# Kernel optimization log

Hardware: AMD Instinct MI355X
Metric: run time of the kernel (lower is better)

Reference implementation:

```python
import jax, jax.numpy as jnp
import numpy as np

N_NODES = 24576
N_EDGES = 294912
B_GRAPHS = 128
D_IN = 92
D = 512
H = 8
HD = D // H
L = 3
DFF = 4 * D
LN_EPS = 1e-5


def _layer_norm(x, g, b):
    mu = jnp.mean(x, axis=-1, keepdims=True)
    var = jnp.mean((x - mu) ** 2, axis=-1, keepdims=True)
    return (x - mu) * jax.lax.rsqrt(var + LN_EPS) * g + b


def setup_inputs() -> dict:
    key = jax.random.key(0)
    ks = jax.random.split(key, 24)
    s = 0.02
    inp = {
        "node_features": jax.random.normal(ks[0], (N_NODES, D_IN), jnp.float32),
        "edge_index": jax.random.randint(ks[1], (2, N_EDGES), 0, N_NODES, jnp.int64),
        "edge_attr": jax.random.uniform(ks[2], (N_EDGES,), jnp.float32),
        "batch": jnp.sort(jax.random.randint(ks[3], (N_NODES,), 0, B_GRAPHS, jnp.int64)),
        # atom embedding Linear(92 -> D)
        "emb_w": jax.random.normal(ks[4], (D, D_IN), jnp.float32) * s,
        "emb_b": jnp.zeros((D,), jnp.float32),
        # per-layer MHA params (stacked over L layers)
        "in_proj_w": jax.random.normal(ks[5], (L, 3 * D, D), jnp.float32) * s,
        "in_proj_b": jnp.zeros((L, 3 * D), jnp.float32),
        "out_w": jax.random.normal(ks[6], (L, D, D), jnp.float32) * s,
        "out_b": jnp.zeros((L, D), jnp.float32),
        "ln1_g": jnp.ones((L, D), jnp.float32),
        "ln1_b": jnp.zeros((L, D), jnp.float32),
        "ffn_w1": jax.random.normal(ks[7], (L, DFF, D), jnp.float32) * s,
        "ffn_b1": jnp.zeros((L, DFF), jnp.float32),
        "ffn_w2": jax.random.normal(ks[8], (L, D, DFF), jnp.float32) * s,
        "ffn_b2": jnp.zeros((L, D), jnp.float32),
        "ln2_g": jnp.ones((L, D), jnp.float32),
        "ln2_b": jnp.zeros((L, D), jnp.float32),
        # output head: Linear(D,D) -> SiLU -> Linear(D,1)
        "head_w1": jax.random.normal(ks[9], (D, D), jnp.float32) * s,
        "head_b1": jnp.zeros((D,), jnp.float32),
        "head_w2": jax.random.normal(ks[10], (1, D), jnp.float32) * s,
        "head_b2": jnp.zeros((1,), jnp.float32),
    }
    return inp


def _forward(node_features, batch, emb_w, emb_b, in_proj_w, in_proj_b, out_w,
             out_b, ln1_g, ln1_b, ffn_w1, ffn_b1, ffn_w2, ffn_b2, ln2_g,
             ln2_b, head_w1, head_b1, head_w2, head_b2):
    N = node_features.shape[0]
    B = int(jnp.max(batch)) + 1
    counts = jnp.bincount(batch, length=B)            # (B,) nodes per graph
    S = int(jnp.max(counts))                          # max_nodes
    starts = jnp.searchsorted(batch, jnp.arange(B))   # batch is sorted
    pos = jnp.arange(N) - starts[batch]               # slot within graph

    h = node_features @ emb_w.T + emb_b               # (N, D)
    # ragged -> dense pad  (B, S, D)
    hp = jnp.zeros((B, S, D), h.dtype).at[batch, pos].set(h)
    key_pad = jnp.arange(S)[None, :] >= counts[:, None]   # True = padding

    scale = 1.0 / jnp.sqrt(jnp.asarray(HD, hp.dtype))
    for l in range(L):
        qkv = hp @ in_proj_w[l].T + in_proj_b[l]      # (B, S, 3D)
        q, k, v = jnp.split(qkv, 3, axis=-1)
        q = q.reshape(B, S, H, HD).transpose(0, 2, 1, 3)
        k = k.reshape(B, S, H, HD).transpose(0, 2, 1, 3)
        v = v.reshape(B, S, H, HD).transpose(0, 2, 1, 3)
        scores = jnp.einsum('bhqd,bhkd->bhqk', q, k) * scale
        scores = jnp.where(key_pad[:, None, None, :], -jnp.inf, scores)
        attn = jax.nn.softmax(scores, axis=-1)
        o = jnp.einsum('bhqk,bhkd->bhqd', attn, v)
        o = o.transpose(0, 2, 1, 3).reshape(B, S, D)
        o = o @ out_w[l].T + out_b[l]
        x = _layer_norm(hp + o, ln1_g[l], ln1_b[l])   # post-norm
        f = jax.nn.relu(x @ ffn_w1[l].T + ffn_b1[l]) @ ffn_w2[l].T + ffn_b2[l]
        hp = _layer_norm(x + f, ln2_g[l], ln2_b[l])

    # unpad + segment mean pool
    h_out = hp[batch, pos]                            # (N, D)
    pooled = jax.ops.segment_sum(h_out, batch, num_segments=B)
    pooled = pooled / counts[:, None].astype(pooled.dtype)
    y = jax.nn.silu(pooled @ head_w1.T + head_b1) @ head_w2.T + head_b2
    return y                                          # (B, 1)


def reference(node_features, edge_index, edge_attr, batch, emb_w, emb_b,
              in_proj_w, in_proj_b, out_w, out_b, ln1_g, ln1_b, ffn_w1,
              ffn_b1, ffn_w2, ffn_b2, ln2_g, ln2_b, head_w1, head_b1,
              head_w2, head_b2):
    # edge_index / edge_attr are accepted but unused, matching the torch forward
    return _forward(node_features, batch, emb_w, emb_b, in_proj_w, in_proj_b,
                    out_w, out_b, ln1_g, ln1_b, ffn_w1, ffn_b1, ffn_w2,
                    ffn_b2, ln2_g, ln2_b, head_w1, head_b1, head_w2, head_b2)
```

## Files before the change

### kernel.cpp

```cpp
#include <hip/hip_runtime.h>
#include <hip/hip_bf16.h>
#include <cstdint>
#include <cfloat>
#include <cstddef>
#include <type_traits>

#define N_NODES 24576
#define B_GRAPHS 128
#define D_IN 92
#define D_INP 96
#define DMODEL 512
#define NHEAD 8
#define HDIM 64
#define NLAYER 3
#define DFF 2048

typedef __attribute__((ext_vector_type(8))) short short8;
typedef __attribute__((ext_vector_type(4))) short short4v;
typedef __attribute__((ext_vector_type(8))) unsigned short ushort8;
typedef __attribute__((ext_vector_type(4))) float f32x4;

__device__ __forceinline__ float b2f(unsigned short u) {
  union { unsigned int i; float f; } x;
  x.i = ((unsigned int)u) << 16;
  return x.f;
}
__device__ __forceinline__ unsigned short f2b(float f) {
  __hip_bfloat16 h = __float2bfloat16(f);
  return *reinterpret_cast<unsigned short*>(&h);
}

__device__ __forceinline__ void gl2lds16(const __hip_bfloat16* g,
                                         __hip_bfloat16* l) {
  __builtin_amdgcn_global_load_lds(
      (const __attribute__((address_space(1))) unsigned int*)g,
      (__attribute__((address_space(3))) unsigned int*)l, 16, 0, 0);
}

__global__ void starts_k(const int* __restrict__ batch32, int* __restrict__ starts) {
  __shared__ int is64_s;
  const int tid = threadIdx.x;
  if (tid == 0) is64_s = 0;
  __syncthreads();
  int bad = 0;
  for (int i = tid; i < N_NODES - 1; i += 256)
    if (batch32[i] > batch32[i + 1]) bad = 1;
  if (bad) atomicOr(&is64_s, 1);
  __syncthreads();
  const int is64 = is64_s;
  if (tid <= B_GRAPHS) {
    int lo = 0, hi = N_NODES;
    while (lo < hi) {
      int mid = (lo + hi) >> 1;
      int v = is64 ? batch32[2 * mid] : batch32[mid];
      if (v < tid) lo = mid + 1; else hi = mid;
    }
    starts[tid] = lo;
  }
}

__global__ __launch_bounds__(256) void cvt_k(const float* __restrict__ in,
                                             __hip_bfloat16* __restrict__ out,
                                             int count4) {
  int i = blockIdx.x * 256 + threadIdx.x;
  if (i < count4) {
    float4 v = ((const float4*)in)[i];
    short4v o;
    o[0] = (short)f2b(v.x); o[1] = (short)f2b(v.y);
    o[2] = (short)f2b(v.z); o[3] = (short)f2b(v.w);
    ((short4v*)out)[i] = o;
  }
}

__global__ __launch_bounds__(256) void padcvt_k(const float* __restrict__ in,
                                                __hip_bfloat16* __restrict__ out,
                                                int rows) {
  int idx = blockIdx.x * 256 + threadIdx.x;
  if (idx < rows * D_INP) {
    int r = idx / D_INP, c = idx - r * D_INP;
    out[idx] = __float2bfloat16(c < D_IN ? in[(size_t)r * D_IN + c] : 0.0f);
  }
}

__global__ __launch_bounds__(256) void mgemm_k(
    const __hip_bfloat16* __restrict__ A, const __hip_bfloat16* __restrict__ W,
    const float* __restrict__ bias, const __hip_bfloat16* __restrict__ res,
    __hip_bfloat16* __restrict__ C, int M, int N, int K, int act) {
  __shared__ __align__(16) __hip_bfloat16 As[3][128 * 32];
  __shared__ __align__(16) __hip_bfloat16 Ws[3][128 * 32];
  const int tid = threadIdx.x;
  const int wave = tid >> 6, lane = tid & 63;

  const int nxt = N >> 7, nmt = M >> 7;
  int rowt, colt;
  if ((nmt & 7) == 0) {
    const int rows_per = nmt >> 3;
    const int x = blockIdx.x & 7;
    const int j = blockIdx.x >> 3;
    rowt = x * rows_per + j % rows_per;
    colt = j / rows_per;
  } else {
    rowt = blockIdx.x / nxt;
    colt = blockIdx.x % nxt;
  }
  const int m0 = rowt * 128, n0 = colt * 128;

  const int mw = (wave >> 1) * 64, nw = (wave & 1) * 64;
  const int quad = lane >> 4, l16 = lane & 15;

  f32x4 acc[4][4] = {};

  const int srow = wave * 32 + (lane >> 2);
  const int skc = (((lane & 3) + ((lane >> 2) >> 1)) & 3) * 8;
  const __hip_bfloat16* gA = A + (size_t)(m0 + srow) * K + skc;
  const __hip_bfloat16* gW = W + (size_t)(n0 + srow) * K + skc;
  const int lo = wave * 32 * 32;

  const int niter = K >> 5;
  gl2lds16(gA, &As[0][lo]);
  gl2lds16(gA + (size_t)16 * K, &As[0][lo + 16 * 32]);
  gl2lds16(gW, &Ws[0][lo]);
  gl2lds16(gW + (size_t)16 * K, &Ws[0][lo + 16 * 32]);
  if (niter > 1) {
    gl2lds16(gA + 32, &As[1][lo]);
    gl2lds16(gA + (size_t)16 * K + 32, &As[1][lo + 16 * 32]);
    gl2lds16(gW + 32, &Ws[1][lo]);
    gl2lds16(gW + (size_t)16 * K + 32, &Ws[1][lo + 16 * 32]);
  }

  const int prd = ((quad - (l16 >> 1)) & 3) * 8;

  for (int it = 0; it < niter; ++it) {
    if (it + 1 < niter)
      asm volatile("s_waitcnt vmcnt(4)\n\ts_barrier" ::: "memory");
    else
      asm volatile("s_waitcnt vmcnt(0)\n\ts_barrier" ::: "memory");
    if (it + 2 < niter) {
      const int kpre = (it + 2) * 32;
      const int nb = (it + 2) % 3;
      gl2lds16(gA + kpre, &As[nb][lo]);
      gl2lds16(gA + (size_t)16 * K + kpre, &As[nb][lo + 16 * 32]);
      gl2lds16(gW + kpre, &Ws[nb][lo]);
      gl2lds16(gW + (size_t)16 * K + kpre, &Ws[nb][lo + 16 * 32]);
    }
    const int cb = it % 3;
    short8 af[4], bf[4];
#pragma unroll
    for (int t = 0; t < 4; t++) {
      af[t] = *(const short8*)&As[cb][(mw + t * 16 + l16) * 32 + prd];
      bf[t] = *(const short8*)&Ws[cb][(nw + t * 16 + l16) * 32 + prd];
    }
#pragma unroll
    for (int mt = 0; mt < 4; mt++)
#pragma unroll
      for (int nt = 0; nt < 4; nt++)
        acc[mt][nt] = __builtin_amdgcn_mfma_f32_16x16x32_bf16(
            af[mt], bf[nt], acc[mt][nt], 0, 0, 0);
  }

  __syncthreads();
  float* eps = ((wave < 2) ? (float*)As : (float*)Ws) + (wave & 1) * (32 * 68);
  const int erow = lane >> 3;
  const int ec = (lane & 7) * 8;
#pragma unroll
  for (int pass = 0; pass < 2; pass++) {
#pragma unroll
    for (int mh = 0; mh < 2; mh++) {
      const int mt = pass * 2 + mh;
#pragma unroll
      for (int nt = 0; nt < 4; nt++) {
        const float bv = bias[n0 + nw + nt * 16 + l16];
#pragma unroll
        for (int i = 0; i < 4; i++)
          eps[(mh * 16 + quad * 4 + i) * 68 + nt * 16 + l16] =
              acc[mt][nt][i] + bv;
      }
    }
    asm volatile("s_waitcnt lgkmcnt(0)" ::: "memory");
#pragma unroll
    for (int j = 0; j < 4; j++) {
      const int r = j * 8 + erow;
      const int m = m0 + mw + pass * 32 + r;
      const int n = n0 + nw + ec;
      f32x4 v0 = *(const f32x4*)&eps[r * 68 + ec];
      f32x4 v1 = *(const f32x4*)&eps[r * 68 + ec + 4];
      float v[8] = {v0[0], v0[1], v0[2], v0[3], v1[0], v1[1], v1[2], v1[3]};
      if (res) {
        ushort8 rv = *(const ushort8*)((const unsigned short*)res +
                                       (size_t)m * N + n);
#pragma unroll
        for (int t = 0; t < 8; t++) v[t] += b2f(rv[t]);
      }
      ushort8 o;
#pragma unroll
      for (int t = 0; t < 8; t++) {
        float x = (act == 1) ? fmaxf(v[t], 0.0f) : v[t];
        o[t] = f2b(x);
      }
      *(ushort8*)((unsigned short*)C + (size_t)m * N + n) = o;
    }
    asm volatile("s_waitcnt lgkmcnt(0)" ::: "memory");
  }
}

__global__ __launch_bounds__(256) void gemm_k(
    const float* __restrict__ A, const float* __restrict__ W,
    const float* __restrict__ bias, const float* __restrict__ res,
    float* __restrict__ C, int M, int N, int K, int act) {
  __shared__ float As[16][68];
  __shared__ float Ws[16][68];
  const int tid = threadIdx.x;
  const int tx = tid & 15, ty = tid >> 4;
  const int m0 = blockIdx.y * 64, n0 = blockIdx.x * 64;
  const int lr = tid >> 2;
  const int lk = (tid & 3) * 4;
  float acc[4][4] = {{0.f}};
  for (int k0 = 0; k0 < K; k0 += 16) {
#pragma unroll
    for (int i = 0; i < 4; i++) {
      int k = k0 + lk + i;
      As[lk + i][lr] = (k < K) ? A[(size_t)(m0 + lr) * K + k] : 0.0f;
      Ws[lk + i][lr] = (k < K) ? W[(size_t)(n0 + lr) * K + k] : 0.0f;
    }
    __syncthreads();
#pragma unroll
    for (int kk = 0; kk < 16; kk++) {
      float4 a4 = *(const float4*)&As[kk][ty * 4];
      float4 w4 = *(const float4*)&Ws[kk][tx * 4];
      float a[4] = {a4.x, a4.y, a4.z, a4.w};
      float w[4] = {w4.x, w4.y, w4.z, w4.w};
#pragma unroll
      for (int i = 0; i < 4; i++)
#pragma unroll
        for (int j = 0; j < 4; j++) acc[i][j] += a[i] * w[j];
    }
    __syncthreads();
  }
#pragma unroll
  for (int i = 0; i < 4; i++) {
    int m = m0 + ty * 4 + i;
#pragma unroll
    for (int j = 0; j < 4; j++) {
      int n = n0 + tx * 4 + j;
      float v = acc[i][j] + bias[n];
      if (res) v += res[(size_t)m * N + n];
      if (act == 1) v = fmaxf(v, 0.0f);
      else if (act == 2) v = v / (1.0f + __expf(-v));
      C[(size_t)m * N + n] = v;
    }
  }
}

__global__ __launch_bounds__(256) void lnb_k(
    const __hip_bfloat16* __restrict__ in, const float* __restrict__ g,
    const float* __restrict__ b, __hip_bfloat16* __restrict__ out) {
  int row = blockIdx.x * 4 + (threadIdx.x >> 6);
  int lane = threadIdx.x & 63;
  const unsigned short* rp =
      (const unsigned short*)in + (size_t)row * DMODEL + lane * 8;
  ushort8 sv = *(const ushort8*)rp;
  float v[8];
  float s = 0.f;
#pragma unroll
  for (int i = 0; i < 8; i++) { v[i] = b2f(sv[i]); s += v[i]; }
#pragma unroll
  for (int off = 32; off; off >>= 1) s += __shfl_xor(s, off);
  float mu = s * (1.0f / DMODEL);
  float vs = 0.f;
#pragma unroll
  for (int i = 0; i < 8; i++) { float d = v[i] - mu; vs += d * d; }
#pragma unroll
  for (int off = 32; off; off >>= 1) vs += __shfl_xor(vs, off);
  float rs = rsqrtf(vs * (1.0f / DMODEL) + 1e-5f);
  ushort8 o;
#pragma unroll
  for (int i = 0; i < 8; i++) {
    int c = lane * 8 + i;
    o[i] = f2b((v[i] - mu) * rs * g[c] + b[c]);
  }
  *(ushort8*)((unsigned short*)out + (size_t)row * DMODEL + lane * 8) = o;
}

#define MAXNH 128
__global__ __launch_bounds__(256, 3) void attn5_k(
    const __hip_bfloat16* __restrict__ qkv, const int* __restrict__ starts,
    __hip_bfloat16* __restrict__ O1, __hip_bfloat16* __restrict__ O2,
    float* __restrict__ ml) {
  const int half = blockIdx.x & 1;
  const int gh = blockIdx.x >> 1;
  const int g = gh >> 3, h = gh & 7;
  int s0 = starts[g], s1 = starts[g + 1];
  s0 = min(max(s0, 0), N_NODES);
  s1 = min(max(s1, s0), N_NODES);
  const int n = s1 - s0, start = s0;
  if (n == 0) return;
  const int tid = threadIdx.x, wave = tid >> 6, lane = tid & 63;
  const int quad = lane >> 4, l16 = lane & 15;
  unsigned short* Oh = (unsigned short*)(half ? O2 : O1);

  __shared__ __align__(16) unsigned short Ks[128][72];
  __shared__ __align__(16) unsigned short Vt[64][136];
  __shared__ __align__(16) unsigned short Ps[4][16][136];

  if (n <= 2 * MAXNH) {
    const int nh1 = (n + 1) >> 1;
    const int k0g = half * nh1;
    const int nh = half ? (n - nh1) : nh1;
    const int ktq = (n + 15) >> 4;

    if (nh == 0) {
      for (int mt = wave; mt < ktq; mt += 4) {
        const int q = mt * 16 + l16;
        if (q < n) {
          short4v z = {0, 0, 0, 0};
#pragma unroll
          for (int dt = 0; dt < 4; dt++)
            *(short4v*)(Oh + (size_t)(start + q) * DMODEL + h * HDIM +
                        dt * 16 + quad * 4) = z;
          if (quad == 0) {
            float2 mlv = {-FLT_MAX, 0.0f};
            *(float2*)(ml + ((size_t)(start + q) * NHEAD + h) * 4 + half * 2) = mlv;
          }
        }
      }
      return;
    }

    for (int idx = tid; idx < nh * 8; idx += 256) {
      int r = idx >> 3, c = (idx & 7) * 8;
      *(ushort8*)&Ks[r][c] = *(const ushort8*)((const unsigned short*)qkv +
                                               (size_t)(start + k0g + r) * 1536 +
                                               512 + h * HDIM + c);
    }
    for (int idx = tid; idx < 16 * 8; idx += 256) {
      int r = nh + (idx >> 3), c = (idx & 7) * 8;
      if (r < 128) {
        ushort8 z = {0, 0, 0, 0, 0, 0, 0, 0};
        *(ushort8*)&Ks[r][c] = z;
      }
    }
    const int vr = tid & 31, dc8 = tid >> 5;
    for (int r0 = 0; r0 < nh; r0 += 32) {
      int r = r0 + vr;
      if (r < nh) {
        ushort8 v = *(const ushort8*)((const unsigned short*)qkv +
                                      (size_t)(start + k0g + r) * 1536 + 1024 +
                                      h * HDIM + dc8 * 8);
#pragma unroll
        for (int j = 0; j < 8; j++) Vt[dc8 * 8 + j][r] = v[j];
      }
    }
    for (int idx = tid; idx < 64 * 32; idx += 256) {
      int d = idx >> 5, r = nh + (idx & 31);
      if (r < 136) Vt[d][r] = 0;
    }
    __syncthreads();

    const int ktmax2 = (nh + 15) >> 4;
    const int nkc2 = (nh + 31) >> 5;
    const float scale = 0.125f;

    for (int mt = wave; mt < ktq; mt += 4) {
      const int qrow = start + min(mt * 16 + l16, n - 1);
      const short8 qf0 = *(const short8*)((const unsigned short*)qkv +
                                          (size_t)qrow * 1536 + h * HDIM + quad * 8);
      const short8 qf1 = *(const short8*)((const unsigned short*)qkv +
                                          (size_t)qrow * 1536 + h * HDIM + 32 + quad * 8);
      f32x4 sacc[8];
#pragma unroll
      for (int kt = 0; kt < 8; kt++) {
        if (kt < ktmax2) {
          const int krow = kt * 16 + l16;
          const short8 kf0 = *(const short8*)&Ks[krow][quad * 8];
          const short8 kf1 = *(const short8*)&Ks[krow][32 + quad * 8];
          f32x4 a = {0.f, 0.f, 0.f, 0.f};
          a = __builtin_amdgcn_mfma_f32_16x16x32_bf16(kf0, qf0, a, 0, 0, 0);
          a = __builtin_amdgcn_mfma_f32_16x16x32_bf16(kf1, qf1, a, 0, 0, 0);
          sacc[kt] = a;
        }
      }
      float mx = -FLT_MAX;
#pragma unroll
      for (int kt = 0; kt < 8; kt++) {
        if (kt < ktmax2) {
#pragma unroll
          for (int i = 0; i < 4; i++) {
            const int key = kt * 16 + quad * 4 + i;
            const float v = sacc[kt][i] * scale;
            sacc[kt][i] = v;
            if (key < nh) mx = fmaxf(mx, v);
          }
        }
      }
      mx = fmaxf(mx, __shfl_xor(mx, 16));
      mx = fmaxf(mx, __shfl_xor(mx, 32));
      float ls = 0.f;
#pragma unroll
      for (int kt = 0; kt < 8; kt++) {
        if (kt < ktmax2) {
#pragma unroll
          for (int i = 0; i < 4; i++) {
            const int key = kt * 16 + quad * 4 + i;
            const float p = (key < nh) ? __expf(sacc[kt][i] - mx) : 0.0f;
            sacc[kt][i] = p;
            ls += p;
          }
        }
      }
      ls += __shfl_xor(ls, 16);
      ls += __shfl_xor(ls, 32);
#pragma unroll
      for (int kt = 0; kt < 8; kt++) {
        if (kt < 2 * nkc2) {
          short4v pp;
#pragma unroll
          for (int i = 0; i < 4; i++) {
            const float p = (kt < ktmax2) ? sacc[kt][i] : 0.0f;
            pp[i] = (short)f2b(p);
          }
          *(short4v*)&Ps[wave][l16][kt * 16 + quad * 4] = pp;
        }
      }
      asm volatile("s_waitcnt lgkmcnt(0)" ::: "memory");
      const int qv = mt * 16 + l16;
#pragma unroll
      for (int dt = 0; dt < 4; dt++) {
        f32x4 oa = {0.f, 0.f, 0.f, 0.f};
#pragma unroll
        for (int kc = 0; kc < 4; kc++) {
          if (kc < nkc2) {
            const short8 vf = *(const short8*)&Vt[dt * 16 + l16][kc * 32 + quad * 8];
            const short8 pf = *(const short8*)&Ps[wave][l16][kc * 32 + quad * 8];
            oa = __builtin_amdgcn_mfma_f32_16x16x32_bf16(vf, pf, oa, 0, 0, 0);
          }
        }
        if (qv < n) {
          short4v ov;
#pragma unroll
          for (int i = 0; i < 4; i++) ov[i] = (short)f2b(oa[i]);
          *(short4v*)(Oh + (size_t)(start + qv) * DMODEL + h * HDIM +
                      dt * 16 + quad * 4) = ov;
        }
      }
      if (qv < n && quad == 0) {
        float2 mlv = {mx, ls};
        *(float2*)(ml + ((size_t)(start + qv) * NHEAD + h) * 4 + half * 2) = mlv;
      }
    }
  } else {
    const float scale = 0.125f;
    int nn = min(n, 512);
    if (half == 1) {
      for (int qi = wave; qi < nn; qi += 4) {
        Oh[(size_t)(start + qi) * DMODEL + h * HDIM + lane] = 0;
        if (lane == 0) {
          float2 mlv = {-FLT_MAX, 0.0f};
          *(float2*)(ml + ((size_t)(start + qi) * NHEAD + h) * 4 + 2) = mlv;
        }
      }
      return;
    }
    for (int qi = wave; qi < nn; qi += 4) {
      float qd = __bfloat162float(
          qkv[(size_t)(start + qi) * (3 * DMODEL) + h * HDIM + lane]);
      float sreg[8];
#pragma unroll
      for (int t = 0; t < 8; t++) {
        float sc = -FLT_MAX;
        if (t * 64 < nn) {
          int k = t * 64 + lane, kc = min(k, nn - 1);
          const __hip_bfloat16* Kr =
              qkv + (size_t)(start + kc) * (3 * DMODEL) + DMODEL + h * HDIM;
          float a = 0.f;
#pragma unroll
          for (int d = 0; d < 64; d++)
            a += __shfl(qd, d) * __bfloat162float(Kr[d]);
          if (k < nn) sc = a * scale;
        }
        sreg[t] = sc;
      }
      float m = -FLT_MAX;
#pragma unroll
      for (int t = 0; t < 8; t++) m = fmaxf(m, sreg[t]);
#pragma unroll
      for (int off = 32; off; off >>= 1) m = fmaxf(m, __shfl_xor(m, off));
      float lsum = 0.f;
#pragma unroll
      for (int t = 0; t < 8; t++) {
        float p = (sreg[t] == -FLT_MAX) ? 0.0f : __expf(sreg[t] - m);
        sreg[t] = p;
        lsum += p;
      }
#pragma unroll
      for (int off = 32; off; off >>= 1) lsum += __shfl_xor(lsum, off);
      float inv_l = 1.0f / lsum;
      float o = 0.f;
#pragma unroll
      for (int t = 0; t < 8; t++) {
        int kb = t * 64;
        if (kb < nn) {
          int kmax = min(64, nn - kb);
          const __hip_bfloat16* Vb = qkv + (size_t)(start + kb) * (3 * DMODEL) +
                                     2 * DMODEL + h * HDIM + lane;
          for (int j = 0; j < kmax; j++)
            o += __shfl(sreg[t], j) *
                 __bfloat162float(Vb[(size_t)j * (3 * DMODEL)]);
        }
      }
      Oh[(size_t)(start + qi) * DMODEL + h * HDIM + lane] = f2b(o * inv_l);
      if (lane == 0) {
        float2 mlv = {0.0f, 1.0f};
        *(float2*)(ml + ((size_t)(start + qi) * NHEAD + h) * 4) = mlv;
      }
    }
  }
}

__global__ __launch_bounds__(256) void merge_k(
    const __hip_bfloat16* __restrict__ O1, const __hip_bfloat16* __restrict__ O2,
    const float* __restrict__ ml, __hip_bfloat16* __restrict__ out) {
  int t = blockIdx.x * 256 + threadIdx.x;
  int node = t >> 6;
  int rem = t & 63;
  int h = rem >> 3;
  int c8 = (rem & 7) * 8;
  float4 m4 = *(const float4*)(ml + ((size_t)node * NHEAD + h) * 4);
  float mm = fmaxf(m4.x, m4.z);
  float w1 = __expf(m4.x - mm), w2 = __expf(m4.z - mm);
  float inv = 1.0f / (w1 * m4.y + w2 * m4.w);
  size_t off = (size_t)node * DMODEL + h * HDIM + c8;
  ushort8 a = *(const ushort8*)((const unsigned short*)O1 + off);
  ushort8 b = *(const ushort8*)((const unsigned short*)O2 + off);
  ushort8 o;
#pragma unroll
  for (int i = 0; i < 8; i++)
    o[i] = f2b((w1 * b2f(a[i]) + w2 * b2f(b[i])) * inv);
  *(ushort8*)((unsigned short*)out + off) = o;
}

__global__ __launch_bounds__(256) void pool_k(
    const __hip_bfloat16* __restrict__ hp, const int* __restrict__ starts,
    float* __restrict__ pooled) {
  int g = blockIdx.x;
  int s0 = starts[g], s1 = starts[g + 1];
  s0 = min(max(s0, 0), N_NODES);
  s1 = min(max(s1, s0), N_NODES);
  int n = s1 - s0;
  float inv = n > 0 ? 1.0f / (float)n : 0.0f;
  int c = blockIdx.y * 256 + threadIdx.x;
  float acc = 0.f;
  for (int r = s0; r < s1; r++)
    acc += __bfloat162float(hp[(size_t)r * DMODEL + c]);
  pooled[(size_t)g * DMODEL + c] = acc * inv;
}

__global__ __launch_bounds__(256) void head2_k(
    const float* __restrict__ h1, const float* __restrict__ w2,
    const float* __restrict__ b2, float* __restrict__ y) {
  int row = blockIdx.x * 4 + (threadIdx.x >> 6);
  int lane = threadIdx.x & 63;
  float s = 0.f;
#pragma unroll
  for (int i = 0; i < 8; i++) {
    int c = lane + i * 64;
    s += h1[(size_t)row * DMODEL + c] * w2[c];
  }
#pragma unroll
  for (int off = 32; off; off >>= 1) s += __shfl_xor(s, off);
  if (lane == 0) y[row] = s + b2[0];
}

extern "C" void kernel_launch(void* const* d_in, const int* in_sizes, int n_in,
                              void* d_out, int out_size, void* d_ws,
                              size_t ws_size, hipStream_t stream) {
  const float* node_features = (const float*)d_in[0];
  const int* batch = (const int*)d_in[3];
  const float* emb_w = (const float*)d_in[4];
  const float* emb_b = (const float*)d_in[5];
  const float* in_proj_w = (const float*)d_in[6];
  const float* in_proj_b = (const float*)d_in[7];
  const float* out_w = (const float*)d_in[8];
  const float* out_b = (const float*)d_in[9];
  const float* ln1_g = (const float*)d_in[10];
  const float* ln1_b = (const float*)d_in[11];
  const float* ffn_w1 = (const float*)d_in[12];
  const float* ffn_b1 = (const float*)d_in[13];
  const float* ffn_w2 = (const float*)d_in[14];
  const float* ffn_b2 = (const float*)d_in[15];
  const float* ln2_g = (const float*)d_in[16];
  const float* ln2_b = (const float*)d_in[17];
  const float* head_w1 = (const float*)d_in[18];
  const float* head_b1 = (const float*)d_in[19];
  const float* head_w2 = (const float*)d_in[20];
  const float* head_b2 = (const float*)d_in[21];
  float* y = (float*)d_out;

  typedef __hip_bfloat16 bf;
  char* wsb = (char*)d_ws;
  int* starts = (int*)wsb;
  bf* nf_b = (bf*)(wsb + 1024);
  bf* wq_b = nf_b + (size_t)N_NODES * D_INP;
  bf* wo_b = wq_b + (size_t)NLAYER * 3 * DMODEL * DMODEL;
  bf* w1_b = wo_b + (size_t)NLAYER * DMODEL * DMODEL;
  bf* w2_b = w1_b + (size_t)NLAYER * DFF * DMODEL;
  bf* we_b = w2_b + (size_t)NLAYER * DMODEL * DFF;
  bf* hp   = we_b + (size_t)DMODEL * D_INP;
  bf* xb   = hp + (size_t)N_NODES * DMODEL;
  bf* t1b  = xb + (size_t)N_NODES * DMODEL;
  bf* qkvb = t1b + (size_t)N_NODES * DMODEL;
  bf* ffh  = qkvb;
  float* pooled = (float*)((char*)ffh + (size_t)N_NODES * DFF * 2);
  float* h1 = pooled + (size_t)B_GRAPHS * DMODEL;
  float* ml = h1 + (size_t)B_GRAPHS * DMODEL;

  starts_k<<<1, 256, 0, stream>>>(batch, starts);

  {
    int c4;
    c4 = NLAYER * 3 * DMODEL * DMODEL / 4;
    cvt_k<<<(c4 + 255) / 256, 256, 0, stream>>>(in_proj_w, wq_b, c4);
    c4 = NLAYER * DMODEL * DMODEL / 4;
    cvt_k<<<(c4 + 255) / 256, 256, 0, stream>>>(out_w, wo_b, c4);
    c4 = NLAYER * DFF * DMODEL / 4;
    cvt_k<<<(c4 + 255) / 256, 256, 0, stream>>>(ffn_w1, w1_b, c4);
    cvt_k<<<(c4 + 255) / 256, 256, 0, stream>>>(ffn_w2, w2_b, c4);
    padcvt_k<<<(N_NODES * D_INP + 255) / 256, 256, 0, stream>>>(node_features,
                                                                nf_b, N_NODES);
    padcvt_k<<<(DMODEL * D_INP + 255) / 256, 256, 0, stream>>>(emb_w, we_b,
                                                               DMODEL);
  }

  mgemm_k<<<(N_NODES / 128) * (DMODEL / 128), 256, 0, stream>>>(
      nf_b, we_b, emb_b, nullptr, hp, N_NODES, DMODEL, D_INP, 0);

  for (int l = 0; l < NLAYER; l++) {
    const bf* wq = wq_b + (size_t)l * 3 * DMODEL * DMODEL;
    const bf* wo = wo_b + (size_t)l * DMODEL * DMODEL;
    const bf* w1 = w1_b + (size_t)l * DFF * DMODEL;
    const bf* w2 = w2_b + (size_t)l * DMODEL * DFF;
    const float* ipb = in_proj_b + (size_t)l * 3 * DMODEL;
    const float* ob = out_b + (size_t)l * DMODEL;
    const float* b1 = ffn_b1 + (size_t)l * DFF;
    const float* b2 = ffn_b2 + (size_t)l * DMODEL;

    mgemm_k<<<(N_NODES / 128) * (3 * DMODEL / 128), 256, 0, stream>>>(
        hp, wq, ipb, nullptr, qkvb, N_NODES, 3 * DMODEL, DMODEL, 0);

    attn5_k<<<B_GRAPHS * NHEAD * 2, 256, 0, stream>>>(qkvb, starts, t1b, xb, ml);
    merge_k<<<N_NODES * 64 / 256, 256, 0, stream>>>(t1b, xb, ml, t1b);

    mgemm_k<<<(N_NODES / 128) * (DMODEL / 128), 256, 0, stream>>>(
        t1b, wo, ob, hp, xb, N_NODES, DMODEL, DMODEL, 0);
    lnb_k<<<N_NODES / 4, 256, 0, stream>>>(xb, ln1_g + l * DMODEL,
                                           ln1_b + l * DMODEL, xb);

    mgemm_k<<<(N_NODES / 128) * (DFF / 128), 256, 0, stream>>>(
        xb, w1, b1, nullptr, ffh, N_NODES, DFF, DMODEL, 1);
    mgemm_k<<<(N_NODES / 128) * (DMODEL / 128), 256, 0, stream>>>(
        ffh, w2, b2, xb, t1b, N_NODES, DMODEL, DFF, 0);

    lnb_k<<<N_NODES / 4, 256, 0, stream>>>(t1b, ln2_g + l * DMODEL,
                                           ln2_b + l * DMODEL, hp);
  }

  pool_k<<<dim3(B_GRAPHS, 2), 256, 0, stream>>>(hp, starts, pooled);
  gemm_k<<<dim3(DMODEL / 64, B_GRAPHS / 64), 256, 0, stream>>>(
      pooled, head_w1, head_b1, nullptr, h1, B_GRAPHS, DMODEL, DMODEL, 2);
  head2_k<<<B_GRAPHS / 4, 256, 0, stream>>>(h1, head_w2, head_b2, y);
}
```

Measured before the change: 1.166 ms.

## Fuse weight/input bf16 conversions into one kernel and prefetch Q fragments in attention

Replaces six separate fp32-to-bf16 conversion launches with a single prep kernel that dispatches by flat index range, and vectorizes the padded node-feature conversion to four elements per thread. Separately, the attention kernel now loads the next query tile's fragments one iteration ahead so global-load latency overlaps the MFMA work. This reduces launch overhead and conversion cost at the price of some branching and extra live registers in attention.

```diff
diff --git a/kernel.cpp b/kernel.cpp
--- a/kernel.cpp
+++ b/kernel.cpp
@@ -59,27 +59,48 @@
   }
 }
 
-__global__ __launch_bounds__(256) void cvt_k(const float* __restrict__ in,
-                                             __hip_bfloat16* __restrict__ out,
-                                             int count4) {
-  int i = blockIdx.x * 256 + threadIdx.x;
-  if (i < count4) {
-    float4 v = ((const float4*)in)[i];
-    short4v o;
-    o[0] = (short)f2b(v.x); o[1] = (short)f2b(v.y);
-    o[2] = (short)f2b(v.z); o[3] = (short)f2b(v.w);
-    ((short4v*)out)[i] = o;
-  }
-}
-
-__global__ __launch_bounds__(256) void padcvt_k(const float* __restrict__ in,
-                                                __hip_bfloat16* __restrict__ out,
-                                                int rows) {
-  int idx = blockIdx.x * 256 + threadIdx.x;
-  if (idx < rows * D_INP) {
-    int r = idx / D_INP, c = idx - r * D_INP;
-    out[idx] = __float2bfloat16(c < D_IN ? in[(size_t)r * D_IN + c] : 0.0f);
-  }
+#define QW0 589824
+#define QW1 196608
+#define QW2 786432
+#define QW3 786432
+#define QP4 589824
+#define QP5 12288
+#define QTOT (QW0 + QW1 + QW2 + QW3 + QP4 + QP5)
+__global__ __launch_bounds__(256) void prep_k(
+    const float* __restrict__ s0, const float* __restrict__ s1,
+    const float* __restrict__ s2, const float* __restrict__ s3,
+    const float* __restrict__ s4, const float* __restrict__ s5,
+    __hip_bfloat16* __restrict__ d0, __hip_bfloat16* __restrict__ d1,
+    __hip_bfloat16* __restrict__ d2, __hip_bfloat16* __restrict__ d3,
+    __hip_bfloat16* __restrict__ d4, __hip_bfloat16* __restrict__ d5) {
+  int q = blockIdx.x * 256 + threadIdx.x;
+  const float* src;
+  __hip_bfloat16* dst;
+  int qi;
+  bool pad = false;
+  if (q < QW0) { src = s0; dst = d0; qi = q; }
+  else if ((q -= QW0) < QW1) { src = s1; dst = d1; qi = q; }
+  else if ((q -= QW1) < QW2) { src = s2; dst = d2; qi = q; }
+  else if ((q -= QW2) < QW3) { src = s3; dst = d3; qi = q; }
+  else if ((q -= QW3) < QP4) { src = s4; dst = d4; qi = q; pad = true; }
+  else if ((q -= QP4) < QP5) { src = s5; dst = d5; qi = q; pad = true; }
+  else return;
+  float4 v;
+  if (!pad) {
+    v = ((const float4*)src)[qi];
+  } else {
+    int r = qi / 24, cq = (qi % 24) * 4;
+    if (cq < 92) {
+      const float* p = src + (size_t)r * D_IN + cq;
+      v = make_float4(p[0], p[1], p[2], p[3]);
+    } else {
+      v = make_float4(0.f, 0.f, 0.f, 0.f);
+    }
+  }
+  short4v o;
+  o[0] = (short)f2b(v.x); o[1] = (short)f2b(v.y);
+  o[2] = (short)f2b(v.z); o[3] = (short)f2b(v.w);
+  ((short4v*)dst)[qi] = o;
 }
 
 __global__ __launch_bounds__(256) void mgemm_k(
@@ -360,12 +381,24 @@
     const int nkc2 = (nh + 31) >> 5;
     const float scale = 0.125f;
 
+    short8 qf0, qf1;
+    if (wave < ktq) {
+      const int qrow = start + min(wave * 16 + l16, n - 1);
+      qf0 = *(const short8*)((const unsigned short*)qkv + (size_t)qrow * 1536 +
+                             h * HDIM + quad * 8);
+      qf1 = *(const short8*)((const unsigned short*)qkv + (size_t)qrow * 1536 +
+                             h * HDIM + 32 + quad * 8);
+    }
+
     for (int mt = wave; mt < ktq; mt += 4) {
-      const int qrow = start + min(mt * 16 + l16, n - 1);
-      const short8 qf0 = *(const short8*)((const unsigned short*)qkv +
-                                          (size_t)qrow * 1536 + h * HDIM + quad * 8);
-      const short8 qf1 = *(const short8*)((const unsigned short*)qkv +
-                                          (size_t)qrow * 1536 + h * HDIM + 32 + quad * 8);
+      const short8 cq0 = qf0, cq1 = qf1;
+      if (mt + 4 < ktq) {
+        const int qrow = start + min((mt + 4) * 16 + l16, n - 1);
+        qf0 = *(const short8*)((const unsigned short*)qkv +
+                               (size_t)qrow * 1536 + h * HDIM + quad * 8);
+        qf1 = *(const short8*)((const unsigned short*)qkv +
+                               (size_t)qrow * 1536 + h * HDIM + 32 + quad * 8);
+      }
       f32x4 sacc[8];
 #pragma unroll
       for (int kt = 0; kt < 8; kt++) {
@@ -374,8 +407,8 @@
           const short8 kf0 = *(const short8*)&Ks[krow][quad * 8];
           const short8 kf1 = *(const short8*)&Ks[krow][32 + quad * 8];
           f32x4 a = {0.f, 0.f, 0.f, 0.f};
-          a = __builtin_amdgcn_mfma_f32_16x16x32_bf16(kf0, qf0, a, 0, 0, 0);
-          a = __builtin_amdgcn_mfma_f32_16x16x32_bf16(kf1, qf1, a, 0, 0, 0);
+          a = __builtin_amdgcn_mfma_f32_16x16x32_bf16(kf0, cq0, a, 0, 0, 0);
+          a = __builtin_amdgcn_mfma_f32_16x16x32_bf16(kf1, cq1, a, 0, 0, 0);
           sacc[kt] = a;
         }
       }
@@ -615,20 +648,9 @@
 
   starts_k<<<1, 256, 0, stream>>>(batch, starts);
 
-  {
-    int c4;
-    c4 = NLAYER * 3 * DMODEL * DMODEL / 4;
-    cvt_k<<<(c4 + 255) / 256, 256, 0, stream>>>(in_proj_w, wq_b, c4);
-    c4 = NLAYER * DMODEL * DMODEL / 4;
-    cvt_k<<<(c4 + 255) / 256, 256, 0, stream>>>(out_w, wo_b, c4);
-    c4 = NLAYER * DFF * DMODEL / 4;
-    cvt_k<<<(c4 + 255) / 256, 256, 0, stream>>>(ffn_w1, w1_b, c4);
-    cvt_k<<<(c4 + 255) / 256, 256, 0, stream>>>(ffn_w2, w2_b, c4);
-    padcvt_k<<<(N_NODES * D_INP + 255) / 256, 256, 0, stream>>>(node_features,
-                                                                nf_b, N_NODES);
-    padcvt_k<<<(DMODEL * D_INP + 255) / 256, 256, 0, stream>>>(emb_w, we_b,
-                                                               DMODEL);
-  }
+  prep_k<<<(QTOT + 255) / 256, 256, 0, stream>>>(
+      in_proj_w, out_w, ffn_w1, ffn_w2, node_features, emb_w,
+      wq_b, wo_b, w1_b, w2_b, nf_b, we_b);
 
   mgemm_k<<<(N_NODES / 128) * (DMODEL / 128), 256, 0, stream>>>(
       nf_b, we_b, emb_b, nullptr, hp, N_NODES, DMODEL, D_INP, 0);
```

New measurement: 1.157 ms. About the same (-0.8%).
